# Kernel tuning notes

Hardware: AMD Instinct MI355X
Metric: run time of the kernel (lower is better)

Reference implementation:

```python
import jax, jax.numpy as jnp
import numpy as np

B, CH, N = 131072, 2, 8  # batch, pos/neg channels, coarse graph size
L1, L2 = 64, 32          # latent_gcn, latent2_gcn
NEG_SLOPE = 0.2


def _row_normalize(a):
    # GCN-style row normalization: D^-1 A, zeroing rows with zero sum
    rowsum = a.sum(-1, keepdims=True)
    r_inv = jnp.where(rowsum > 0, 1.0 / rowsum, 0.0)
    return a * r_inv


def _leaky(x):
    return jnp.where(x >= 0, x, NEG_SLOPE * x)


def setup_inputs() -> dict:
    key = jax.random.key(0)
    ks = jax.random.split(key, 16)
    u = lambda k, shape, s: jax.random.uniform(k, shape, jnp.float32, -s, s)
    s1 = 1.0 / np.sqrt(L1)
    s2 = 1.0 / np.sqrt(L2)
    d_in = CH * N * L2            # 512
    d_h1 = N * N                  # 64
    d_h2 = int(N * N * 0.5)       # 32
    return {
        "adj": jax.random.uniform(ks[0], (B, CH, N, N), jnp.float32),
        "Wp1": u(ks[1], (N, L1), s1),  "bp1": u(ks[2], (L1,), s1),
        "Wp2": u(ks[3], (L1, L2), s2), "bp2": u(ks[4], (L2,), s2),
        "Wn1": u(ks[5], (N, L1), s1),  "bn1": u(ks[6], (L1,), s1),
        "Wn2": u(ks[7], (L1, L2), s2), "bn2": u(ks[8], (L2,), s2),
        "Wl1": u(ks[9], (d_in, d_h1), 1.0 / np.sqrt(d_in)),  "bl1": u(ks[10], (d_h1,), 1.0 / np.sqrt(d_in)),
        "Wl2": u(ks[11], (d_h1, d_h2), 1.0 / np.sqrt(d_h1)), "bl2": u(ks[12], (d_h2,), 1.0 / np.sqrt(d_h1)),
        "Wl3": u(ks[13], (d_h2, 1), 1.0 / np.sqrt(d_h2)),    "bl3": u(ks[14], (1,), 1.0 / np.sqrt(d_h2)),
    }


def reference(adj, Wp1, bp1, Wp2, bp2, Wn1, bn1, Wn2, bn2,
              Wl1, bl1, Wl2, bl2, Wl3, bl3):
    # adj: [B, 2, N, N]; channel 0 -> positive GCN, channel 1 -> negative GCN
    Ap = _row_normalize(adj[:, 0])  # [B, N, N]
    An = _row_normalize(adj[:, 1])

    # input features x = eye(N), so eye @ W == W; keep general via broadcast
    def gcn2(A, W1, b1, W2, b2):
        x1 = _leaky(jnp.einsum('bij,jk->bik', A, W1) + b1)        # [B, N, L1]
        x2 = _leaky(jnp.einsum('bij,bjk->bik', A, x1 @ W2) + b2)  # [B, N, L2]
        return x2

    xp = gcn2(Ap, Wp1, bp1, Wp2, bp2)
    xn = gcn2(An, Wn1, bn1, Wn2, bn2)
    x_ = jnp.stack([xp, xn], axis=1)          # [B, 2, N, L2]
    x = x_.reshape(x_.shape[0], -1)           # [B, 2*N*L2]

    h = _leaky(x @ Wl1 + bl1)
    h = _leaky(h @ Wl2 + bl2)
    return h @ Wl3 + bl3                      # [B, 1]
```

## Files before the change

### kernel.cpp

```cpp
#include <hip/hip_runtime.h>

typedef _Float16 f16;
typedef _Float16 f16x2 __attribute__((ext_vector_type(2)));
typedef _Float16 f16x4 __attribute__((ext_vector_type(4)));
typedef _Float16 f16x8 __attribute__((ext_vector_type(8)));
typedef float    f32x4 __attribute__((ext_vector_type(4)));
typedef unsigned int u32;
typedef u32      u32x2 __attribute__((ext_vector_type(2)));
typedef u32      u32x4 __attribute__((ext_vector_type(4)));

#define MFMA32(a, b, c) __builtin_amdgcn_mfma_f32_16x16x32_f16((a), (b), (c), 0, 0, 0)
#define MFMA16(a, b, c) __builtin_amdgcn_mfma_f32_16x16x16f16((a), (b), (c), 0, 0, 0)

__device__ __forceinline__ float leaky(float x) {
    return fmaf(0.4f, __builtin_fabsf(x), 0.6f * x);
}
__device__ __forceinline__ u32 pkrtz(float a, float b) {
    return __builtin_bit_cast(u32, __builtin_amdgcn_cvt_pkrtz(a, b));
}
__device__ __forceinline__ u32 lk_pk2(float a, float b) {
    f16x2 v = __builtin_bit_cast(f16x2, __builtin_amdgcn_cvt_pkrtz(a, b));
    f16x2 z2 = {(f16)0.0f, (f16)0.0f};
    f16x2 mx = __builtin_elementwise_max(v, z2);
    f16x2 mn = __builtin_elementwise_min(v, z2);
    f16x2 r = mn * (f16x2){(f16)0.2f, (f16)0.2f} + mx;
    return __builtin_bit_cast(u32, r);
}
__device__ __forceinline__ f16x4 lk_pk4(const f32x4 z) {
    return __builtin_bit_cast(f16x4, (u32x2){ lk_pk2(z[0], z[1]), lk_pk2(z[2], z[3]) });
}
__device__ __forceinline__ f16x4 pk4(const f32x4 z) {
    return __builtin_bit_cast(f16x4, (u32x2){ pkrtz(z[0], z[1]), pkrtz(z[2], z[3]) });
}
__device__ __forceinline__ void st_lk4(void* p, const f32x4 z) {
    *(u32x2*)p = (u32x2){ lk_pk2(z[0], z[1]), lk_pk2(z[2], z[3]) };
}

__global__ void disc_prepack(const float* __restrict__ Wp1, const float* __restrict__ Wp2,
                             const float* __restrict__ Wn1, const float* __restrict__ Wn2,
                             const float* __restrict__ Wl1, const float* __restrict__ Wl2,
                             f16* __restrict__ ws)
{
    int idx = blockIdx.x * 256 + threadIdx.x;
    if (idx >= 84 * 512 + 24 * 256) return;
    float v = 0.0f;
    if (idx < 84 * 512) {
        int f = idx >> 9, r = idx & 511;
        int lane = r >> 3, e = r & 7;
        int m15 = lane & 15, h = lane >> 4;
        if (f < 64) {
            int mt4 = f >> 4, ks4 = f & 15;
            int k = ks4 * 32 + h * 8 + e;
            v = Wl1[k * 64 + mt4 * 16 + m15];
        } else if (f < 72) {
            int q = f - 64, c = q >> 2, mt = q & 3;
            const float* W1 = c ? Wn1 : Wp1;
            v = (lane < 16) ? W1[e * 64 + mt * 16 + m15] : 0.0f;
        } else if (f < 80) {
            int q = f - 72, c = q >> 2, nt2 = (q >> 1) & 1, ks2 = q & 1;
            const float* W2 = c ? Wn2 : Wp2;
            int k = ks2 * 32 + h * 8 + e;
            v = W2[k * 32 + nt2 * 16 + m15];
        } else {
            int q = f - 80, ms5 = q >> 1, ks5 = q & 1;
            int k = ks5 * 32 + h * 8 + e;
            v = Wl2[k * 32 + ms5 * 16 + m15];
        }
    } else {
        int r2 = idx - 84 * 512;
        int f2 = r2 >> 8, rr = r2 & 255;
        int lane = rr >> 2, e = rr & 3;
        int m15 = lane & 15, h = lane >> 4;
        if (f2 < 16) {
            int c = f2 >> 3, kb = (f2 >> 1) & 3, nt = f2 & 1;
            const float* W2 = c ? Wn2 : Wp2;
            v = W2[(kb * 16 + h * 4 + e) * 32 + nt * 16 + m15];
        } else {
            int q = f2 - 16, kb = q >> 1, nt = q & 1;
            v = Wl2[(kb * 16 + h * 4 + e) * 32 + nt * 16 + m15];
        }
    }
    ws[idx] = (f16)v;
}

__global__ __launch_bounds__(128, 2) void disc_main(
    const float* __restrict__ adj,
    const float* __restrict__ bp1, const float* __restrict__ bp2,
    const float* __restrict__ bn1, const float* __restrict__ bn2,
    const float* __restrict__ bl1, const float* __restrict__ bl2,
    const float* __restrict__ bl3, const float* __restrict__ Wl3,
    const f16* __restrict__ ws, float* __restrict__ out)
{
    extern __shared__ char smem[];
    const int tid  = threadIdx.x;
    const int lane = tid & 63;
    const int wid  = tid >> 6;
    const int h    = lane >> 4;
    const int m15  = lane & 15;
    const int i7   = lane & 7;
    const int r8   = m15 >> 3;

    const f16x8* wsf = (const f16x8*)ws;
    const f16x4* wsq = (const f16x4*)(ws + 84 * 512);
    const int c = wid;

    const f16x8* w1p = wsf + (64 + c * 4) * 64 + lane;
    f16x8 w1t0 = w1p[0], w1t1 = w1p[64], w1t2 = w1p[128], w1t3 = w1p[192];
    const f16x4* w2p = wsq + (c * 8) * 64 + lane;
    f16x4 w2k00 = w2p[0],   w2k01 = w2p[64];
    f16x4 w2k10 = w2p[128], w2k11 = w2p[192];
    f16x4 w2k20 = w2p[256], w2k21 = w2p[320];
    f16x4 w2k30 = w2p[384], w2k31 = w2p[448];
    const f32x4* b1p = (const f32x4*)(c ? bn1 : bp1);
    f32x4 b10 = b1p[h], b11 = b1p[4 + h], b12 = b1p[8 + h], b13 = b1p[12 + h];
    const f32x4* b2p = (const f32x4*)(c ? bn2 : bp2);
    f32x4 b20 = b2p[h], b21 = b2p[4 + h];
    f32x4 bl1v0 = ((const f32x4*)bl1)[h],      bl1v1 = ((const f32x4*)bl1)[4 + h];
    f32x4 bl1v2 = ((const f32x4*)bl1)[8 + h],  bl1v3 = ((const f32x4*)bl1)[12 + h];

    char* wbase = smem + wid * 10240;
    char* Albuf = wbase;
    char* xbuf  = wbase + 2048;
    char* xchg  = smem + 10240;

    const long b0 = (long)blockIdx.x * 16;
    const int rxor = ((m15 >> 1) & 3) << 4;
    const bool bsel = ((h >> 1) == r8);
    const int  hlow = h & 1;
    f32x4 zero4 = {0.0f, 0.0f, 0.0f, 0.0f};
    f16x4 zf4 = {};

    f32x4 a40 = wid ? zero4 : bl1v0;
    f32x4 a41 = wid ? zero4 : bl1v1;
    f32x4 a42 = wid ? zero4 : bl1v2;
    f32x4 a43 = wid ? zero4 : bl1v3;

    #pragma unroll
    for (int q = 0; q < 2; ++q) {
        int rid = q * 64 + lane;
        const f32x4* rp = (const f32x4*)(adj + (b0 + (rid >> 3)) * 128 + c * 64 + (rid & 7) * 8);
        f32x4 a0 = rp[0];
        f32x4 a1 = rp[1];
        float s = ((a0[0] + a0[1]) + (a0[2] + a0[3])) + ((a1[0] + a1[1]) + (a1[2] + a1[3]));
        float rv = (s > 0.0f) ? (1.0f / s) : 0.0f;
        f16x8 row;
        row[0] = (f16)(a0[0] * rv); row[1] = (f16)(a0[1] * rv);
        row[2] = (f16)(a0[2] * rv); row[3] = (f16)(a0[3] * rv);
        row[4] = (f16)(a1[0] * rv); row[5] = (f16)(a1[1] * rv);
        row[6] = (f16)(a1[2] * rv); row[7] = (f16)(a1[3] * rv);
        *(f16x8*)(Albuf + rid * 16) = row;
    }

    #pragma unroll 1
    for (int tp = 0; tp < 4; ++tp) {
        const int ta = tp, tb = tp + 4;
        f16x8 arow_a = *(const f16x8*)(Albuf + (((2 * ta + r8) * 8 + i7) << 4));
        f16x8 arow_b = *(const f16x8*)(Albuf + (((2 * tb + r8) * 8 + i7) << 4));

        f32x4 z0a = MFMA32(w1t0, arow_a, b10);
        f32x4 z1a = MFMA32(w1t1, arow_a, b11);
        f32x4 z2a = MFMA32(w1t2, arow_a, b12);
        f32x4 z3a = MFMA32(w1t3, arow_a, b13);
        f32x4 z0b = MFMA32(w1t0, arow_b, b10);
        f32x4 z1b = MFMA32(w1t1, arow_b, b11);
        f32x4 z2b = MFMA32(w1t2, arow_b, b12);
        f32x4 z3b = MFMA32(w1t3, arow_b, b13);

        f16x4 xa0 = lk_pk4(z0a), xa1 = lk_pk4(z1a), xa2 = lk_pk4(z2a), xa3 = lk_pk4(z3a);
        f16x4 xb0 = lk_pk4(z0b), xb1 = lk_pk4(z1b), xb2 = lk_pk4(z2b), xb3 = lk_pk4(z3b);

        f32x4 y0a = MFMA16(xa0, w2k00, zero4);
        f32x4 y1a = MFMA16(xa0, w2k01, zero4);
        f32x4 y0b = MFMA16(xb0, w2k00, zero4);
        f32x4 y1b = MFMA16(xb0, w2k01, zero4);
        y0a = MFMA16(xa1, w2k10, y0a);
        y1a = MFMA16(xa1, w2k11, y1a);
        y0b = MFMA16(xb1, w2k10, y0b);
        y1b = MFMA16(xb1, w2k11, y1b);
        y0a = MFMA16(xa2, w2k20, y0a);
        y1a = MFMA16(xa2, w2k21, y1a);
        y0b = MFMA16(xb2, w2k20, y0b);
        y1b = MFMA16(xb2, w2k21, y1b);
        y0a = MFMA16(xa3, w2k30, y0a);
        y1a = MFMA16(xa3, w2k31, y1a);
        y0b = MFMA16(xb3, w2k30, y0b);
        y1b = MFMA16(xb3, w2k31, y1b);

        f16x4 pa0 = pk4(y0a), pa1 = pk4(y1a);
        f16x4 pb0 = pk4(y0b), pb1 = pk4(y1b);
        u32x4 ara = __builtin_bit_cast(u32x4, arow_a);
        u32x4 arb = __builtin_bit_cast(u32x4, arow_b);
        f16x4 halfa = __builtin_bit_cast(f16x4,
            hlow ? (u32x2){ara[2], ara[3]} : (u32x2){ara[0], ara[1]});
        f16x4 halfb = __builtin_bit_cast(f16x4,
            hlow ? (u32x2){arb[2], arb[3]} : (u32x2){arb[0], arb[1]});
        f16x4 bfra = bsel ? halfa : zf4;
        f16x4 bfrb = bsel ? halfb : zf4;

        f32x4 x2aa = MFMA16(pa0, bfra, b20);
        f32x4 x2ba = MFMA16(pa1, bfra, b21);
        f32x4 x2ab = MFMA16(pb0, bfrb, b20);
        f32x4 x2bb = MFMA16(pb1, bfrb, b21);

        const int lga = h >> 1;
        const int lgb = (lga + 2) & 3;
        char* fb = xbuf + (i7 << 10);
        {
            int wx = ((ta & 3) ^ i7) << 4;
            int basew = ((2 * ta + r8) << 6) + ((h & 1) << 3);
            st_lk4(fb + ((basew + lga * 16) ^ wx), x2aa);
            st_lk4(fb + ((basew + lgb * 16) ^ wx), x2ba);
        }
        {
            int wx = ((tb & 3) ^ i7) << 4;
            int basew = ((2 * tb + r8) << 6) + ((h & 1) << 3);
            st_lk4(fb + ((basew + lga * 16) ^ wx), x2ab);
            st_lk4(fb + ((basew + lgb * 16) ^ wx), x2bb);
        }
    }

    __builtin_amdgcn_s_setprio(1);
    #pragma unroll 4
    for (int k8 = 0; k8 < 8; ++k8) {
        int xr = rxor ^ (k8 << 4);
        f16x8 xf = *(const f16x8*)(xbuf + (k8 << 10) + ((m15 * 64 + h * 16) ^ xr));
        const f16x8* wl = wsf + (c * 8 + k8) * 64 + lane;
        a40 = MFMA32(wl[0],    xf, a40);
        a41 = MFMA32(wl[1024], xf, a41);
        a42 = MFMA32(wl[2048], xf, a42);
        a43 = MFMA32(wl[3072], xf, a43);
    }
    __builtin_amdgcn_s_setprio(0);

    if (wid == 1) {
        *(f32x4*)(xchg +    0 + lane * 16) = a40;
        *(f32x4*)(xchg + 1024 + lane * 16) = a41;
        *(f32x4*)(xchg + 2048 + lane * 16) = a42;
        *(f32x4*)(xchg + 3072 + lane * 16) = a43;
    }
    __syncthreads();
    if (wid == 0) {
        a40 += *(const f32x4*)(xchg +    0 + lane * 16);
        a41 += *(const f32x4*)(xchg + 1024 + lane * 16);
        a42 += *(const f32x4*)(xchg + 2048 + lane * 16);
        a43 += *(const f32x4*)(xchg + 3072 + lane * 16);

        f16x4 pd0 = lk_pk4(a40), pd1 = lk_pk4(a41);
        f16x4 pd2 = lk_pk4(a42), pd3 = lk_pk4(a43);

        const f16x4* wl2p = wsq + 16 * 64 + lane;
        f16x4 l200 = wl2p[0],   l201 = wl2p[64];
        f16x4 l210 = wl2p[128], l211 = wl2p[192];
        f16x4 l220 = wl2p[256], l221 = wl2p[320];
        f16x4 l230 = wl2p[384], l231 = wl2p[448];
        float c0 = bl2[m15], c1 = bl2[m15 + 16];
        f32x4 a50 = {c0, c0, c0, c0};
        f32x4 a51 = {c1, c1, c1, c1};
        a50 = MFMA16(pd0, l200, a50);
        a51 = MFMA16(pd0, l201, a51);
        a50 = MFMA16(pd1, l210, a50);
        a51 = MFMA16(pd1, l211, a51);
        a50 = MFMA16(pd2, l220, a50);
        a51 = MFMA16(pd2, l221, a51);
        a50 = MFMA16(pd3, l230, a50);
        a51 = MFMA16(pd3, l231, a51);

        float w30 = Wl3[m15], w31 = Wl3[m15 + 16];
        const float bl3s = bl3[0];
        #pragma unroll
        for (int r = 0; r < 4; ++r) {
            float acc = leaky(a50[r]) * w30 + leaky(a51[r]) * w31;
            acc += __shfl_xor(acc, 1);
            acc += __shfl_xor(acc, 2);
            acc += __shfl_xor(acc, 4);
            acc += __shfl_xor(acc, 8);
            if (m15 == 0) out[b0 + h * 4 + r] = acc + bl3s;
        }
    }
}

extern "C" void kernel_launch(void* const* d_in, const int* in_sizes, int n_in,
                              void* d_out, int out_size, void* d_ws, size_t ws_size,
                              hipStream_t stream)
{
    const float* adj  = (const float*)d_in[0];
    const float* Wp1  = (const float*)d_in[1];
    const float* bp1  = (const float*)d_in[2];
    const float* Wp2  = (const float*)d_in[3];
    const float* bp2  = (const float*)d_in[4];
    const float* Wn1  = (const float*)d_in[5];
    const float* bn1  = (const float*)d_in[6];
    const float* Wn2  = (const float*)d_in[7];
    const float* bn2  = (const float*)d_in[8];
    const float* Wl1  = (const float*)d_in[9];
    const float* bl1  = (const float*)d_in[10];
    const float* Wl2  = (const float*)d_in[11];
    const float* bl2  = (const float*)d_in[12];
    const float* Wl3  = (const float*)d_in[13];
    const float* bl3  = (const float*)d_in[14];
    f16* ws = (f16*)d_ws;
    float* out = (float*)d_out;

    hipLaunchKernelGGL(disc_prepack, dim3(192), dim3(256), 0, stream,
                       Wp1, Wp2, Wn1, Wn2, Wl1, Wl2, ws);

    const int ldsBytes = 20480;
    hipFuncSetAttribute(reinterpret_cast<const void*>(disc_main),
                        hipFuncAttributeMaxDynamicSharedMemorySize, ldsBytes);
    hipLaunchKernelGGL(disc_main, dim3(8192), dim3(128), ldsBytes, stream,
                       adj, bp1, bp2, bn1, bn2, bl1, bl2, bl3, Wl3, ws, out);
}
```

Before: 54.74 us.

## Split each channel's work across two waves with four-way cross-wave reduction

Doubles the block to 256 threads so each adjacency channel is handled by two waves. Each wave normalizes half the rows, runs half the GCN tiles and does half of the K-loop of the first dense layer. Partial accumulators from three waves are then reduced through LDS by wave 0. This adds two extra barriers and more LDS reduction traffic in exchange for more waves in flight and shorter per-wave serial chains. The reciprocal is also switched to the hardware rcp approximation.

```diff
diff --git a/kernel.cpp b/kernel.cpp
--- a/kernel.cpp
+++ b/kernel.cpp
@@ -83,7 +83,7 @@
     ws[idx] = (f16)v;
 }
 
-__global__ __launch_bounds__(128, 2) void disc_main(
+__global__ __launch_bounds__(256, 8) void disc_main(
     const float* __restrict__ adj,
     const float* __restrict__ bp1, const float* __restrict__ bp2,
     const float* __restrict__ bn1, const float* __restrict__ bn2,
@@ -95,6 +95,8 @@
     const int tid  = threadIdx.x;
     const int lane = tid & 63;
     const int wid  = tid >> 6;
+    const int c    = wid >> 1;
+    const int half = wid & 1;
     const int h    = lane >> 4;
     const int m15  = lane & 15;
     const int i7   = lane & 7;
@@ -102,7 +104,6 @@
 
     const f16x8* wsf = (const f16x8*)ws;
     const f16x4* wsq = (const f16x4*)(ws + 84 * 512);
-    const int c = wid;
 
     const f16x8* w1p = wsf + (64 + c * 4) * 64 + lane;
     f16x8 w1t0 = w1p[0], w1t1 = w1p[64], w1t2 = w1p[128], w1t3 = w1p[192];
@@ -115,13 +116,10 @@
     f32x4 b10 = b1p[h], b11 = b1p[4 + h], b12 = b1p[8 + h], b13 = b1p[12 + h];
     const f32x4* b2p = (const f32x4*)(c ? bn2 : bp2);
     f32x4 b20 = b2p[h], b21 = b2p[4 + h];
-    f32x4 bl1v0 = ((const f32x4*)bl1)[h],      bl1v1 = ((const f32x4*)bl1)[4 + h];
-    f32x4 bl1v2 = ((const f32x4*)bl1)[8 + h],  bl1v3 = ((const f32x4*)bl1)[12 + h];
-
-    char* wbase = smem + wid * 10240;
-    char* Albuf = wbase;
-    char* xbuf  = wbase + 2048;
-    char* xchg  = smem + 10240;
+
+    char* Albuf = smem + wid * 1024;
+    char* xbuf  = smem + 4096 + c * 8192;
+    char* xchg  = smem;
 
     const long b0 = (long)blockIdx.x * 16;
     const int rxor = ((m15 >> 1) & 3) << 4;
@@ -130,32 +128,28 @@
     f32x4 zero4 = {0.0f, 0.0f, 0.0f, 0.0f};
     f16x4 zf4 = {};
 
-    f32x4 a40 = wid ? zero4 : bl1v0;
-    f32x4 a41 = wid ? zero4 : bl1v1;
-    f32x4 a42 = wid ? zero4 : bl1v2;
-    f32x4 a43 = wid ? zero4 : bl1v3;
-
-    #pragma unroll
-    for (int q = 0; q < 2; ++q) {
-        int rid = q * 64 + lane;
+    {
+        const int rid = half * 64 + lane;
         const f32x4* rp = (const f32x4*)(adj + (b0 + (rid >> 3)) * 128 + c * 64 + (rid & 7) * 8);
         f32x4 a0 = rp[0];
         f32x4 a1 = rp[1];
         float s = ((a0[0] + a0[1]) + (a0[2] + a0[3])) + ((a1[0] + a1[1]) + (a1[2] + a1[3]));
-        float rv = (s > 0.0f) ? (1.0f / s) : 0.0f;
+        float rv = (s > 0.0f) ? __builtin_amdgcn_rcpf(s) : 0.0f;
         f16x8 row;
         row[0] = (f16)(a0[0] * rv); row[1] = (f16)(a0[1] * rv);
         row[2] = (f16)(a0[2] * rv); row[3] = (f16)(a0[3] * rv);
         row[4] = (f16)(a1[0] * rv); row[5] = (f16)(a1[1] * rv);
         row[6] = (f16)(a1[2] * rv); row[7] = (f16)(a1[3] * rv);
-        *(f16x8*)(Albuf + rid * 16) = row;
+        *(f16x8*)(Albuf + lane * 16) = row;
     }
 
     #pragma unroll 1
-    for (int tp = 0; tp < 4; ++tp) {
-        const int ta = tp, tb = tp + 4;
-        f16x8 arow_a = *(const f16x8*)(Albuf + (((2 * ta + r8) * 8 + i7) << 4));
-        f16x8 arow_b = *(const f16x8*)(Albuf + (((2 * tb + r8) * 8 + i7) << 4));
+    for (int tp = 0; tp < 2; ++tp) {
+        const int tla = tp, tlb = tp + 2;
+        const int ta = half * 4 + tla;
+        const int tb = half * 4 + tlb;
+        f16x8 arow_a = *(const f16x8*)(Albuf + (((2 * tla + r8) * 8 + i7) << 4));
+        f16x8 arow_b = *(const f16x8*)(Albuf + (((2 * tlb + r8) * 8 + i7) << 4));
 
         f32x4 z0a = MFMA32(w1t0, arow_a, b10);
         f32x4 z1a = MFMA32(w1t1, arow_a, b11);
@@ -219,9 +213,20 @@
         }
     }
 
+    __syncthreads();
+
+    f32x4 a40 = zero4, a41 = zero4, a42 = zero4, a43 = zero4;
+    if (wid == 0) {
+        a40 = ((const f32x4*)bl1)[h];
+        a41 = ((const f32x4*)bl1)[4 + h];
+        a42 = ((const f32x4*)bl1)[8 + h];
+        a43 = ((const f32x4*)bl1)[12 + h];
+    }
     __builtin_amdgcn_s_setprio(1);
-    #pragma unroll 4
-    for (int k8 = 0; k8 < 8; ++k8) {
+    const int kbase = half * 4;
+    #pragma unroll
+    for (int kq = 0; kq < 4; ++kq) {
+        const int k8 = kbase + kq;
         int xr = rxor ^ (k8 << 4);
         f16x8 xf = *(const f16x8*)(xbuf + (k8 << 10) + ((m15 * 64 + h * 16) ^ xr));
         const f16x8* wl = wsf + (c * 8 + k8) * 64 + lane;
@@ -232,18 +237,24 @@
     }
     __builtin_amdgcn_s_setprio(0);
 
-    if (wid == 1) {
-        *(f32x4*)(xchg +    0 + lane * 16) = a40;
-        *(f32x4*)(xchg + 1024 + lane * 16) = a41;
-        *(f32x4*)(xchg + 2048 + lane * 16) = a42;
-        *(f32x4*)(xchg + 3072 + lane * 16) = a43;
+    __syncthreads();
+    if (wid) {
+        char* dst = xchg + (wid - 1) * 4096 + lane * 16;
+        *(f32x4*)(dst +    0) = a40;
+        *(f32x4*)(dst + 1024) = a41;
+        *(f32x4*)(dst + 2048) = a42;
+        *(f32x4*)(dst + 3072) = a43;
     }
     __syncthreads();
     if (wid == 0) {
-        a40 += *(const f32x4*)(xchg +    0 + lane * 16);
-        a41 += *(const f32x4*)(xchg + 1024 + lane * 16);
-        a42 += *(const f32x4*)(xchg + 2048 + lane * 16);
-        a43 += *(const f32x4*)(xchg + 3072 + lane * 16);
+        #pragma unroll
+        for (int p = 0; p < 3; ++p) {
+            const f32x4* xp = (const f32x4*)(xchg + p * 4096 + lane * 16);
+            a40 += xp[0];
+            a41 += xp[64];
+            a42 += xp[128];
+            a43 += xp[192];
+        }
 
         f16x4 pd0 = lk_pk4(a40), pd1 = lk_pk4(a41);
         f16x4 pd2 = lk_pk4(a42), pd3 = lk_pk4(a43);
@@ -307,6 +318,6 @@
     const int ldsBytes = 20480;
     hipFuncSetAttribute(reinterpret_cast<const void*>(disc_main),
                         hipFuncAttributeMaxDynamicSharedMemorySize, ldsBytes);
-    hipLaunchKernelGGL(disc_main, dim3(8192), dim3(128), ldsBytes, stream,
+    hipLaunchKernelGGL(disc_main, dim3(8192), dim3(256), ldsBytes, stream,
                        adj, bp1, bp2, bn1, bn2, bl1, bl2, bl3, Wl3, ws, out);
 }
```

Result: slower. 175.6 us (+220.9%).

## Make blocks persistent over 8 tiles with register prefetch of next adjacency tile

Applied to the files above, without the earlier changes.

Each block now processes 8 batch tiles of 16 in a loop instead of one, loading the next tile's adjacency rows into registers while the current tile's GCN and MLP compute runs. Per-block weight and bias loads, including the final-layer weights now hoisted out of the loop, are amortised over more work. The exchange buffer moves to its own LDS region and a second barrier is added to protect it between tiles. The grid shrinks to 1024 blocks, so fewer waves are available to hide latency. Reciprocal uses the fast rcp intrinsic.

```diff
diff --git a/kernel.cpp b/kernel.cpp
--- a/kernel.cpp
+++ b/kernel.cpp
@@ -11,6 +11,8 @@
 
 #define MFMA32(a, b, c) __builtin_amdgcn_mfma_f32_16x16x32_f16((a), (b), (c), 0, 0, 0)
 #define MFMA16(a, b, c) __builtin_amdgcn_mfma_f32_16x16x16f16((a), (b), (c), 0, 0, 0)
+
+#define TILES 8
 
 __device__ __forceinline__ float leaky(float x) {
     return fmaf(0.4f, __builtin_fabsf(x), 0.6f * x);
@@ -118,164 +120,204 @@
     f32x4 bl1v0 = ((const f32x4*)bl1)[h],      bl1v1 = ((const f32x4*)bl1)[4 + h];
     f32x4 bl1v2 = ((const f32x4*)bl1)[8 + h],  bl1v3 = ((const f32x4*)bl1)[12 + h];
 
+    f16x4 l200, l201, l210, l211, l220, l221, l230, l231;
+    float c0 = 0.0f, c1 = 0.0f, w30 = 0.0f, w31 = 0.0f, bl3s = 0.0f;
+    if (wid == 0) {
+        const f16x4* wl2p = wsq + 16 * 64 + lane;
+        l200 = wl2p[0];   l201 = wl2p[64];
+        l210 = wl2p[128]; l211 = wl2p[192];
+        l220 = wl2p[256]; l221 = wl2p[320];
+        l230 = wl2p[384]; l231 = wl2p[448];
+        c0 = bl2[m15]; c1 = bl2[m15 + 16];
+        w30 = Wl3[m15]; w31 = Wl3[m15 + 16];
+        bl3s = bl3[0];
+    }
+
     char* wbase = smem + wid * 10240;
     char* Albuf = wbase;
     char* xbuf  = wbase + 2048;
-    char* xchg  = smem + 10240;
-
-    const long b0 = (long)blockIdx.x * 16;
+    char* xchg  = smem + 20480;
+
     const int rxor = ((m15 >> 1) & 3) << 4;
     const bool bsel = ((h >> 1) == r8);
     const int  hlow = h & 1;
     f32x4 zero4 = {0.0f, 0.0f, 0.0f, 0.0f};
     f16x4 zf4 = {};
 
-    f32x4 a40 = wid ? zero4 : bl1v0;
-    f32x4 a41 = wid ? zero4 : bl1v1;
-    f32x4 a42 = wid ? zero4 : bl1v2;
-    f32x4 a43 = wid ? zero4 : bl1v3;
-
-    #pragma unroll
-    for (int q = 0; q < 2; ++q) {
-        int rid = q * 64 + lane;
-        const f32x4* rp = (const f32x4*)(adj + (b0 + (rid >> 3)) * 128 + c * 64 + (rid & 7) * 8);
-        f32x4 a0 = rp[0];
-        f32x4 a1 = rp[1];
-        float s = ((a0[0] + a0[1]) + (a0[2] + a0[3])) + ((a1[0] + a1[1]) + (a1[2] + a1[3]));
-        float rv = (s > 0.0f) ? (1.0f / s) : 0.0f;
-        f16x8 row;
-        row[0] = (f16)(a0[0] * rv); row[1] = (f16)(a0[1] * rv);
-        row[2] = (f16)(a0[2] * rv); row[3] = (f16)(a0[3] * rv);
-        row[4] = (f16)(a1[0] * rv); row[5] = (f16)(a1[1] * rv);
-        row[6] = (f16)(a1[2] * rv); row[7] = (f16)(a1[3] * rv);
-        *(f16x8*)(Albuf + rid * 16) = row;
+    long b0 = (long)blockIdx.x * (16 * TILES);
+
+    f32x4 c00, c01, c10, c11;
+    {
+        const f32x4* rp0 = (const f32x4*)(adj + (b0 + (lane >> 3)) * 128 + c * 64 + (lane & 7) * 8);
+        c00 = rp0[0]; c01 = rp0[1];
+        const int rid1 = 64 + lane;
+        const f32x4* rp1 = (const f32x4*)(adj + (b0 + (rid1 >> 3)) * 128 + c * 64 + (rid1 & 7) * 8);
+        c10 = rp1[0]; c11 = rp1[1];
     }
 
     #pragma unroll 1
-    for (int tp = 0; tp < 4; ++tp) {
-        const int ta = tp, tb = tp + 4;
-        f16x8 arow_a = *(const f16x8*)(Albuf + (((2 * ta + r8) * 8 + i7) << 4));
-        f16x8 arow_b = *(const f16x8*)(Albuf + (((2 * tb + r8) * 8 + i7) << 4));
-
-        f32x4 z0a = MFMA32(w1t0, arow_a, b10);
-        f32x4 z1a = MFMA32(w1t1, arow_a, b11);
-        f32x4 z2a = MFMA32(w1t2, arow_a, b12);
-        f32x4 z3a = MFMA32(w1t3, arow_a, b13);
-        f32x4 z0b = MFMA32(w1t0, arow_b, b10);
-        f32x4 z1b = MFMA32(w1t1, arow_b, b11);
-        f32x4 z2b = MFMA32(w1t2, arow_b, b12);
-        f32x4 z3b = MFMA32(w1t3, arow_b, b13);
-
-        f16x4 xa0 = lk_pk4(z0a), xa1 = lk_pk4(z1a), xa2 = lk_pk4(z2a), xa3 = lk_pk4(z3a);
-        f16x4 xb0 = lk_pk4(z0b), xb1 = lk_pk4(z1b), xb2 = lk_pk4(z2b), xb3 = lk_pk4(z3b);
-
-        f32x4 y0a = MFMA16(xa0, w2k00, zero4);
-        f32x4 y1a = MFMA16(xa0, w2k01, zero4);
-        f32x4 y0b = MFMA16(xb0, w2k00, zero4);
-        f32x4 y1b = MFMA16(xb0, w2k01, zero4);
-        y0a = MFMA16(xa1, w2k10, y0a);
-        y1a = MFMA16(xa1, w2k11, y1a);
-        y0b = MFMA16(xb1, w2k10, y0b);
-        y1b = MFMA16(xb1, w2k11, y1b);
-        y0a = MFMA16(xa2, w2k20, y0a);
-        y1a = MFMA16(xa2, w2k21, y1a);
-        y0b = MFMA16(xb2, w2k20, y0b);
-        y1b = MFMA16(xb2, w2k21, y1b);
-        y0a = MFMA16(xa3, w2k30, y0a);
-        y1a = MFMA16(xa3, w2k31, y1a);
-        y0b = MFMA16(xb3, w2k30, y0b);
-        y1b = MFMA16(xb3, w2k31, y1b);
-
-        f16x4 pa0 = pk4(y0a), pa1 = pk4(y1a);
-        f16x4 pb0 = pk4(y0b), pb1 = pk4(y1b);
-        u32x4 ara = __builtin_bit_cast(u32x4, arow_a);
-        u32x4 arb = __builtin_bit_cast(u32x4, arow_b);
-        f16x4 halfa = __builtin_bit_cast(f16x4,
-            hlow ? (u32x2){ara[2], ara[3]} : (u32x2){ara[0], ara[1]});
-        f16x4 halfb = __builtin_bit_cast(f16x4,
-            hlow ? (u32x2){arb[2], arb[3]} : (u32x2){arb[0], arb[1]});
-        f16x4 bfra = bsel ? halfa : zf4;
-        f16x4 bfrb = bsel ? halfb : zf4;
-
-        f32x4 x2aa = MFMA16(pa0, bfra, b20);
-        f32x4 x2ba = MFMA16(pa1, bfra, b21);
-        f32x4 x2ab = MFMA16(pb0, bfrb, b20);
-        f32x4 x2bb = MFMA16(pb1, bfrb, b21);
-
-        const int lga = h >> 1;
-        const int lgb = (lga + 2) & 3;
-        char* fb = xbuf + (i7 << 10);
+    for (int it = 0; it < TILES; ++it, b0 += 16) {
         {
-            int wx = ((ta & 3) ^ i7) << 4;
-            int basew = ((2 * ta + r8) << 6) + ((h & 1) << 3);
-            st_lk4(fb + ((basew + lga * 16) ^ wx), x2aa);
-            st_lk4(fb + ((basew + lgb * 16) ^ wx), x2ba);
+            float s = ((c00[0] + c00[1]) + (c00[2] + c00[3])) + ((c01[0] + c01[1]) + (c01[2] + c01[3]));
+            float rv = (s > 0.0f) ? __builtin_amdgcn_rcpf(s) : 0.0f;
+            f16x8 row;
+            row[0] = (f16)(c00[0] * rv); row[1] = (f16)(c00[1] * rv);
+            row[2] = (f16)(c00[2] * rv); row[3] = (f16)(c00[3] * rv);
+            row[4] = (f16)(c01[0] * rv); row[5] = (f16)(c01[1] * rv);
+            row[6] = (f16)(c01[2] * rv); row[7] = (f16)(c01[3] * rv);
+            *(f16x8*)(Albuf + lane * 16) = row;
         }
         {
-            int wx = ((tb & 3) ^ i7) << 4;
-            int basew = ((2 * tb + r8) << 6) + ((h & 1) << 3);
-            st_lk4(fb + ((basew + lga * 16) ^ wx), x2ab);
-            st_lk4(fb + ((basew + lgb * 16) ^ wx), x2bb);
-        }
-    }
-
-    __builtin_amdgcn_s_setprio(1);
-    #pragma unroll 4
-    for (int k8 = 0; k8 < 8; ++k8) {
-        int xr = rxor ^ (k8 << 4);
-        f16x8 xf = *(const f16x8*)(xbuf + (k8 << 10) + ((m15 * 64 + h * 16) ^ xr));
-        const f16x8* wl = wsf + (c * 8 + k8) * 64 + lane;
-        a40 = MFMA32(wl[0],    xf, a40);
-        a41 = MFMA32(wl[1024], xf, a41);
-        a42 = MFMA32(wl[2048], xf, a42);
-        a43 = MFMA32(wl[3072], xf, a43);
-    }
-    __builtin_amdgcn_s_setprio(0);
-
-    if (wid == 1) {
-        *(f32x4*)(xchg +    0 + lane * 16) = a40;
-        *(f32x4*)(xchg + 1024 + lane * 16) = a41;
-        *(f32x4*)(xchg + 2048 + lane * 16) = a42;
-        *(f32x4*)(xchg + 3072 + lane * 16) = a43;
-    }
-    __syncthreads();
-    if (wid == 0) {
-        a40 += *(const f32x4*)(xchg +    0 + lane * 16);
-        a41 += *(const f32x4*)(xchg + 1024 + lane * 16);
-        a42 += *(const f32x4*)(xchg + 2048 + lane * 16);
-        a43 += *(const f32x4*)(xchg + 3072 + lane * 16);
-
-        f16x4 pd0 = lk_pk4(a40), pd1 = lk_pk4(a41);
-        f16x4 pd2 = lk_pk4(a42), pd3 = lk_pk4(a43);
-
-        const f16x4* wl2p = wsq + 16 * 64 + lane;
-        f16x4 l200 = wl2p[0],   l201 = wl2p[64];
-        f16x4 l210 = wl2p[128], l211 = wl2p[192];
-        f16x4 l220 = wl2p[256], l221 = wl2p[320];
-        f16x4 l230 = wl2p[384], l231 = wl2p[448];
-        float c0 = bl2[m15], c1 = bl2[m15 + 16];
-        f32x4 a50 = {c0, c0, c0, c0};
-        f32x4 a51 = {c1, c1, c1, c1};
-        a50 = MFMA16(pd0, l200, a50);
-        a51 = MFMA16(pd0, l201, a51);
-        a50 = MFMA16(pd1, l210, a50);
-        a51 = MFMA16(pd1, l211, a51);
-        a50 = MFMA16(pd2, l220, a50);
-        a51 = MFMA16(pd2, l221, a51);
-        a50 = MFMA16(pd3, l230, a50);
-        a51 = MFMA16(pd3, l231, a51);
-
-        float w30 = Wl3[m15], w31 = Wl3[m15 + 16];
-        const float bl3s = bl3[0];
-        #pragma unroll
-        for (int r = 0; r < 4; ++r) {
-            float acc = leaky(a50[r]) * w30 + leaky(a51[r]) * w31;
-            acc += __shfl_xor(acc, 1);
-            acc += __shfl_xor(acc, 2);
-            acc += __shfl_xor(acc, 4);
-            acc += __shfl_xor(acc, 8);
-            if (m15 == 0) out[b0 + h * 4 + r] = acc + bl3s;
-        }
+            float s = ((c10[0] + c10[1]) + (c10[2] + c10[3])) + ((c11[0] + c11[1]) + (c11[2] + c11[3]));
+            float rv = (s > 0.0f) ? __builtin_amdgcn_rcpf(s) : 0.0f;
+            f16x8 row;
+            row[0] = (f16)(c10[0] * rv); row[1] = (f16)(c10[1] * rv);
+            row[2] = (f16)(c10[2] * rv); row[3] = (f16)(c10[3] * rv);
+            row[4] = (f16)(c11[0] * rv); row[5] = (f16)(c11[1] * rv);
+            row[6] = (f16)(c11[2] * rv); row[7] = (f16)(c11[3] * rv);
+            *(f16x8*)(Albuf + (64 + lane) * 16) = row;
+        }
+
+        f32x4 n00, n01, n10, n11;
+        const bool more = (it + 1 < TILES);
+        if (more) {
+            const f32x4* rp0 = (const f32x4*)(adj + (b0 + 16 + (lane >> 3)) * 128 + c * 64 + (lane & 7) * 8);
+            n00 = rp0[0]; n01 = rp0[1];
+            const int rid1 = 64 + lane;
+            const f32x4* rp1 = (const f32x4*)(adj + (b0 + 16 + (rid1 >> 3)) * 128 + c * 64 + (rid1 & 7) * 8);
+            n10 = rp1[0]; n11 = rp1[1];
+        }
+
+        #pragma unroll 1
+        for (int tp = 0; tp < 4; ++tp) {
+            const int ta = tp, tb = tp + 4;
+            f16x8 arow_a = *(const f16x8*)(Albuf + (((2 * ta + r8) * 8 + i7) << 4));
+            f16x8 arow_b = *(const f16x8*)(Albuf + (((2 * tb + r8) * 8 + i7) << 4));
+
+            f32x4 z0a = MFMA32(w1t0, arow_a, b10);
+            f32x4 z1a = MFMA32(w1t1, arow_a, b11);
+            f32x4 z2a = MFMA32(w1t2, arow_a, b12);
+            f32x4 z3a = MFMA32(w1t3, arow_a, b13);
+            f32x4 z0b = MFMA32(w1t0, arow_b, b10);
+            f32x4 z1b = MFMA32(w1t1, arow_b, b11);
+            f32x4 z2b = MFMA32(w1t2, arow_b, b12);
+            f32x4 z3b = MFMA32(w1t3, arow_b, b13);
+
+            f16x4 xa0 = lk_pk4(z0a), xa1 = lk_pk4(z1a), xa2 = lk_pk4(z2a), xa3 = lk_pk4(z3a);
+            f16x4 xb0 = lk_pk4(z0b), xb1 = lk_pk4(z1b), xb2 = lk_pk4(z2b), xb3 = lk_pk4(z3b);
+
+            f32x4 y0a = MFMA16(xa0, w2k00, zero4);
+            f32x4 y1a = MFMA16(xa0, w2k01, zero4);
+            f32x4 y0b = MFMA16(xb0, w2k00, zero4);
+            f32x4 y1b = MFMA16(xb0, w2k01, zero4);
+            y0a = MFMA16(xa1, w2k10, y0a);
+            y1a = MFMA16(xa1, w2k11, y1a);
+            y0b = MFMA16(xb1, w2k10, y0b);
+            y1b = MFMA16(xb1, w2k11, y1b);
+            y0a = MFMA16(xa2, w2k20, y0a);
+            y1a = MFMA16(xa2, w2k21, y1a);
+            y0b = MFMA16(xb2, w2k20, y0b);
+            y1b = MFMA16(xb2, w2k21, y1b);
+            y0a = MFMA16(xa3, w2k30, y0a);
+            y1a = MFMA16(xa3, w2k31, y1a);
+            y0b = MFMA16(xb3, w2k30, y0b);
+            y1b = MFMA16(xb3, w2k31, y1b);
+
+            f16x4 pa0 = pk4(y0a), pa1 = pk4(y1a);
+            f16x4 pb0 = pk4(y0b), pb1 = pk4(y1b);
+            u32x4 ara = __builtin_bit_cast(u32x4, arow_a);
+            u32x4 arb = __builtin_bit_cast(u32x4, arow_b);
+            f16x4 halfa = __builtin_bit_cast(f16x4,
+                hlow ? (u32x2){ara[2], ara[3]} : (u32x2){ara[0], ara[1]});
+            f16x4 halfb = __builtin_bit_cast(f16x4,
+                hlow ? (u32x2){arb[2], arb[3]} : (u32x2){arb[0], arb[1]});
+            f16x4 bfra = bsel ? halfa : zf4;
+            f16x4 bfrb = bsel ? halfb : zf4;
+
+            f32x4 x2aa = MFMA16(pa0, bfra, b20);
+            f32x4 x2ba = MFMA16(pa1, bfra, b21);
+            f32x4 x2ab = MFMA16(pb0, bfrb, b20);
+            f32x4 x2bb = MFMA16(pb1, bfrb, b21);
+
+            const int lga = h >> 1;
+            const int lgb = (lga + 2) & 3;
+            char* fb = xbuf + (i7 << 10);
+            {
+                int wx = ((ta & 3) ^ i7) << 4;
+                int basew = ((2 * ta + r8) << 6) + ((h & 1) << 3);
+                st_lk4(fb + ((basew + lga * 16) ^ wx), x2aa);
+                st_lk4(fb + ((basew + lgb * 16) ^ wx), x2ba);
+            }
+            {
+                int wx = ((tb & 3) ^ i7) << 4;
+                int basew = ((2 * tb + r8) << 6) + ((h & 1) << 3);
+                st_lk4(fb + ((basew + lga * 16) ^ wx), x2ab);
+                st_lk4(fb + ((basew + lgb * 16) ^ wx), x2bb);
+            }
+        }
+
+        f32x4 a40 = wid ? zero4 : bl1v0;
+        f32x4 a41 = wid ? zero4 : bl1v1;
+        f32x4 a42 = wid ? zero4 : bl1v2;
+        f32x4 a43 = wid ? zero4 : bl1v3;
+        __builtin_amdgcn_s_setprio(1);
+        #pragma unroll 4
+        for (int k8 = 0; k8 < 8; ++k8) {
+            int xr = rxor ^ (k8 << 4);
+            f16x8 xf = *(const f16x8*)(xbuf + (k8 << 10) + ((m15 * 64 + h * 16) ^ xr));
+            const f16x8* wl = wsf + (c * 8 + k8) * 64 + lane;
+            a40 = MFMA32(wl[0],    xf, a40);
+            a41 = MFMA32(wl[1024], xf, a41);
+            a42 = MFMA32(wl[2048], xf, a42);
+            a43 = MFMA32(wl[3072], xf, a43);
+        }
+        __builtin_amdgcn_s_setprio(0);
+
+        if (wid == 1) {
+            *(f32x4*)(xchg +    0 + lane * 16) = a40;
+            *(f32x4*)(xchg + 1024 + lane * 16) = a41;
+            *(f32x4*)(xchg + 2048 + lane * 16) = a42;
+            *(f32x4*)(xchg + 3072 + lane * 16) = a43;
+        }
+        __syncthreads();
+        f32x4 p0, p1, p2, p3;
+        if (wid == 0) {
+            p0 = *(const f32x4*)(xchg +    0 + lane * 16);
+            p1 = *(const f32x4*)(xchg + 1024 + lane * 16);
+            p2 = *(const f32x4*)(xchg + 2048 + lane * 16);
+            p3 = *(const f32x4*)(xchg + 3072 + lane * 16);
+        }
+        __syncthreads();
+
+        if (wid == 0) {
+            a40 += p0; a41 += p1; a42 += p2; a43 += p3;
+
+            f16x4 pd0 = lk_pk4(a40), pd1 = lk_pk4(a41);
+            f16x4 pd2 = lk_pk4(a42), pd3 = lk_pk4(a43);
+
+            f32x4 a50 = {c0, c0, c0, c0};
+            f32x4 a51 = {c1, c1, c1, c1};
+            a50 = MFMA16(pd0, l200, a50);
+            a51 = MFMA16(pd0, l201, a51);
+            a50 = MFMA16(pd1, l210, a50);
+            a51 = MFMA16(pd1, l211, a51);
+            a50 = MFMA16(pd2, l220, a50);
+            a51 = MFMA16(pd2, l221, a51);
+            a50 = MFMA16(pd3, l230, a50);
+            a51 = MFMA16(pd3, l231, a51);
+
+            #pragma unroll
+            for (int r = 0; r < 4; ++r) {
+                float acc = leaky(a50[r]) * w30 + leaky(a51[r]) * w31;
+                acc += __shfl_xor(acc, 1);
+                acc += __shfl_xor(acc, 2);
+                acc += __shfl_xor(acc, 4);
+                acc += __shfl_xor(acc, 8);
+                if (m15 == 0) out[b0 + h * 4 + r] = acc + bl3s;
+            }
+        }
+
+        if (more) { c00 = n00; c01 = n01; c10 = n10; c11 = n11; }
     }
 }
 
@@ -304,9 +346,9 @@
     hipLaunchKernelGGL(disc_prepack, dim3(192), dim3(256), 0, stream,
                        Wp1, Wp2, Wn1, Wn2, Wl1, Wl2, ws);
 
-    const int ldsBytes = 20480;
+    const int ldsBytes = 24576;
     hipFuncSetAttribute(reinterpret_cast<const void*>(disc_main),
                         hipFuncAttributeMaxDynamicSharedMemorySize, ldsBytes);
-    hipLaunchKernelGGL(disc_main, dim3(8192), dim3(128), ldsBytes, stream,
+    hipLaunchKernelGGL(disc_main, dim3(8192 / TILES), dim3(128), ldsBytes, stream,
                        adj, bp1, bp2, bn1, bn2, bl1, bl2, bl3, Wl3, ws, out);
 }
```

Result: no change. 54.37 us (-0.7%).

## Use single-wave blocks processing both channels over four batch tiles

Applied to the files above, without the earlier changes.

Restructures the main kernel from two-wave blocks (one wave per channel, combined through LDS and a barrier) to one wave that processes both channels sequentially and loops over four 16-sample tiles. All weights and biases, including the second dense layer, are loaded into registers once per block. This removes the cross-wave exchange and the __syncthreads, and also switches to rcp and a cheaper max-based leaky relu. The catch is much higher register pressure from holding both channels' weights, serial channel processing within a wave, and a grid of only 2048 single-wave blocks, which may reduce latency hiding.

```diff
diff --git a/kernel.cpp b/kernel.cpp
--- a/kernel.cpp
+++ b/kernel.cpp
@@ -12,6 +12,8 @@
 #define MFMA32(a, b, c) __builtin_amdgcn_mfma_f32_16x16x32_f16((a), (b), (c), 0, 0, 0)
 #define MFMA16(a, b, c) __builtin_amdgcn_mfma_f32_16x16x16f16((a), (b), (c), 0, 0, 0)
 
+#define TILES 4
+
 __device__ __forceinline__ float leaky(float x) {
     return fmaf(0.4f, __builtin_fabsf(x), 0.6f * x);
 }
@@ -20,10 +22,8 @@
 }
 __device__ __forceinline__ u32 lk_pk2(float a, float b) {
     f16x2 v = __builtin_bit_cast(f16x2, __builtin_amdgcn_cvt_pkrtz(a, b));
-    f16x2 z2 = {(f16)0.0f, (f16)0.0f};
-    f16x2 mx = __builtin_elementwise_max(v, z2);
-    f16x2 mn = __builtin_elementwise_min(v, z2);
-    f16x2 r = mn * (f16x2){(f16)0.2f, (f16)0.2f} + mx;
+    f16x2 s = v * (f16x2){(f16)0.2f, (f16)0.2f};
+    f16x2 r = __builtin_elementwise_max(v, s);
     return __builtin_bit_cast(u32, r);
 }
 __device__ __forceinline__ f16x4 lk_pk4(const f32x4 z) {
@@ -83,7 +83,7 @@
     ws[idx] = (f16)v;
 }
 
-__global__ __launch_bounds__(128, 2) void disc_main(
+__global__ __launch_bounds__(64, 2) void disc_main(
     const float* __restrict__ adj,
     const float* __restrict__ bp1, const float* __restrict__ bp2,
     const float* __restrict__ bn1, const float* __restrict__ bn2,
@@ -92,9 +92,7 @@
     const f16* __restrict__ ws, float* __restrict__ out)
 {
     extern __shared__ char smem[];
-    const int tid  = threadIdx.x;
-    const int lane = tid & 63;
-    const int wid  = tid >> 6;
+    const int lane = threadIdx.x;
     const int h    = lane >> 4;
     const int m15  = lane & 15;
     const int i7   = lane & 7;
@@ -102,158 +100,152 @@
 
     const f16x8* wsf = (const f16x8*)ws;
     const f16x4* wsq = (const f16x4*)(ws + 84 * 512);
-    const int c = wid;
-
-    const f16x8* w1p = wsf + (64 + c * 4) * 64 + lane;
-    f16x8 w1t0 = w1p[0], w1t1 = w1p[64], w1t2 = w1p[128], w1t3 = w1p[192];
-    const f16x4* w2p = wsq + (c * 8) * 64 + lane;
-    f16x4 w2k00 = w2p[0],   w2k01 = w2p[64];
-    f16x4 w2k10 = w2p[128], w2k11 = w2p[192];
-    f16x4 w2k20 = w2p[256], w2k21 = w2p[320];
-    f16x4 w2k30 = w2p[384], w2k31 = w2p[448];
-    const f32x4* b1p = (const f32x4*)(c ? bn1 : bp1);
-    f32x4 b10 = b1p[h], b11 = b1p[4 + h], b12 = b1p[8 + h], b13 = b1p[12 + h];
-    const f32x4* b2p = (const f32x4*)(c ? bn2 : bp2);
-    f32x4 b20 = b2p[h], b21 = b2p[4 + h];
+
+    const f16x8* w1pp = wsf + 64 * 64 + lane;
+    f16x8 Wp10 = w1pp[0], Wp11 = w1pp[64], Wp12 = w1pp[128], Wp13 = w1pp[192];
+    const f16x4* w2pp = wsq + lane;
+    f16x4 Kp00 = w2pp[0],   Kp01 = w2pp[64];
+    f16x4 Kp10 = w2pp[128], Kp11 = w2pp[192];
+    f16x4 Kp20 = w2pp[256], Kp21 = w2pp[320];
+    f16x4 Kp30 = w2pp[384], Kp31 = w2pp[448];
+    const f32x4* b1pp = (const f32x4*)bp1;
+    f32x4 Bp10 = b1pp[h], Bp11 = b1pp[4 + h], Bp12 = b1pp[8 + h], Bp13 = b1pp[12 + h];
+    const f32x4* b2pp = (const f32x4*)bp2;
+    f32x4 Bp20 = b2pp[h], Bp21 = b2pp[4 + h];
+
+    const f16x8* w1pn = wsf + (64 + 4) * 64 + lane;
+    f16x8 Wn10 = w1pn[0], Wn11 = w1pn[64], Wn12 = w1pn[128], Wn13 = w1pn[192];
+    const f16x4* w2pn = wsq + 8 * 64 + lane;
+    f16x4 Kn00 = w2pn[0],   Kn01 = w2pn[64];
+    f16x4 Kn10 = w2pn[128], Kn11 = w2pn[192];
+    f16x4 Kn20 = w2pn[256], Kn21 = w2pn[320];
+    f16x4 Kn30 = w2pn[384], Kn31 = w2pn[448];
+    const f32x4* b1pn = (const f32x4*)bn1;
+    f32x4 Bn10 = b1pn[h], Bn11 = b1pn[4 + h], Bn12 = b1pn[8 + h], Bn13 = b1pn[12 + h];
+    const f32x4* b2pn = (const f32x4*)bn2;
+    f32x4 Bn20 = b2pn[h], Bn21 = b2pn[4 + h];
+
     f32x4 bl1v0 = ((const f32x4*)bl1)[h],      bl1v1 = ((const f32x4*)bl1)[4 + h];
     f32x4 bl1v2 = ((const f32x4*)bl1)[8 + h],  bl1v3 = ((const f32x4*)bl1)[12 + h];
-
-    char* wbase = smem + wid * 10240;
-    char* Albuf = wbase;
-    char* xbuf  = wbase + 2048;
-    char* xchg  = smem + 10240;
-
-    const long b0 = (long)blockIdx.x * 16;
+    const f16x4* wl2p = wsq + 16 * 64 + lane;
+    f16x4 l200 = wl2p[0],   l201 = wl2p[64];
+    f16x4 l210 = wl2p[128], l211 = wl2p[192];
+    f16x4 l220 = wl2p[256], l221 = wl2p[320];
+    f16x4 l230 = wl2p[384], l231 = wl2p[448];
+    float c0 = bl2[m15], c1 = bl2[m15 + 16];
+    float w30 = Wl3[m15], w31 = Wl3[m15 + 16];
+    const float bl3s = bl3[0];
+
+    char* Albuf = smem;
+    char* xbuf  = smem + 2048;
+
     const int rxor = ((m15 >> 1) & 3) << 4;
     const bool bsel = ((h >> 1) == r8);
     const int  hlow = h & 1;
     f32x4 zero4 = {0.0f, 0.0f, 0.0f, 0.0f};
     f16x4 zf4 = {};
 
-    f32x4 a40 = wid ? zero4 : bl1v0;
-    f32x4 a41 = wid ? zero4 : bl1v1;
-    f32x4 a42 = wid ? zero4 : bl1v2;
-    f32x4 a43 = wid ? zero4 : bl1v3;
-
-    #pragma unroll
-    for (int q = 0; q < 2; ++q) {
-        int rid = q * 64 + lane;
-        const f32x4* rp = (const f32x4*)(adj + (b0 + (rid >> 3)) * 128 + c * 64 + (rid & 7) * 8);
-        f32x4 a0 = rp[0];
-        f32x4 a1 = rp[1];
-        float s = ((a0[0] + a0[1]) + (a0[2] + a0[3])) + ((a1[0] + a1[1]) + (a1[2] + a1[3]));
-        float rv = (s > 0.0f) ? (1.0f / s) : 0.0f;
-        f16x8 row;
-        row[0] = (f16)(a0[0] * rv); row[1] = (f16)(a0[1] * rv);
-        row[2] = (f16)(a0[2] * rv); row[3] = (f16)(a0[3] * rv);
-        row[4] = (f16)(a1[0] * rv); row[5] = (f16)(a1[1] * rv);
-        row[6] = (f16)(a1[2] * rv); row[7] = (f16)(a1[3] * rv);
-        *(f16x8*)(Albuf + rid * 16) = row;
-    }
+    auto run_channel = [&](long b0, int c,
+        f16x8 W10, f16x8 W11, f16x8 W12, f16x8 W13,
+        f16x4 K00, f16x4 K01, f16x4 K10, f16x4 K11,
+        f16x4 K20, f16x4 K21, f16x4 K30, f16x4 K31,
+        f32x4 B10, f32x4 B11, f32x4 B12, f32x4 B13,
+        f32x4 B20, f32x4 B21,
+        f32x4& a40, f32x4& a41, f32x4& a42, f32x4& a43)
+    {
+        {
+            const f32x4* rp0 = (const f32x4*)(adj + (b0 + (lane >> 3)) * 128 + c * 64 + (lane & 7) * 8);
+            const f32x4* rp1 = (const f32x4*)(adj + (b0 + 8 + (lane >> 3)) * 128 + c * 64 + (lane & 7) * 8);
+            f32x4 a0 = rp0[0], a1 = rp0[1];
+            f32x4 b0v = rp1[0], b1v = rp1[1];
+            {
+                float s = ((a0[0] + a0[1]) + (a0[2] + a0[3])) + ((a1[0] + a1[1]) + (a1[2] + a1[3]));
+                float rv = (s > 0.0f) ? __builtin_amdgcn_rcpf(s) : 0.0f;
+                u32x4 row = { pkrtz(a0[0] * rv, a0[1] * rv), pkrtz(a0[2] * rv, a0[3] * rv),
+                              pkrtz(a1[0] * rv, a1[1] * rv), pkrtz(a1[2] * rv, a1[3] * rv) };
+                *(u32x4*)(Albuf + lane * 16) = row;
+            }
+            {
+                float s = ((b0v[0] + b0v[1]) + (b0v[2] + b0v[3])) + ((b1v[0] + b1v[1]) + (b1v[2] + b1v[3]));
+                float rv = (s > 0.0f) ? __builtin_amdgcn_rcpf(s) : 0.0f;
+                u32x4 row = { pkrtz(b0v[0] * rv, b0v[1] * rv), pkrtz(b0v[2] * rv, b0v[3] * rv),
+                              pkrtz(b1v[0] * rv, b1v[1] * rv), pkrtz(b1v[2] * rv, b1v[3] * rv) };
+                *(u32x4*)(Albuf + (64 + lane) * 16) = row;
+            }
+        }
+
+        #pragma unroll
+        for (int t = 0; t < 8; ++t) {
+            f16x8 arow = *(const f16x8*)(Albuf + (((2 * t + r8) * 8 + i7) << 4));
+
+            f32x4 z0 = MFMA32(W10, arow, B10);
+            f32x4 z1 = MFMA32(W11, arow, B11);
+            f32x4 z2 = MFMA32(W12, arow, B12);
+            f32x4 z3 = MFMA32(W13, arow, B13);
+
+            f16x4 x0 = lk_pk4(z0), x1 = lk_pk4(z1), x2 = lk_pk4(z2), x3 = lk_pk4(z3);
+
+            f32x4 y0 = MFMA16(x0, K00, zero4);
+            f32x4 y1 = MFMA16(x0, K01, zero4);
+            y0 = MFMA16(x1, K10, y0);
+            y1 = MFMA16(x1, K11, y1);
+            y0 = MFMA16(x2, K20, y0);
+            y1 = MFMA16(x2, K21, y1);
+            y0 = MFMA16(x3, K30, y0);
+            y1 = MFMA16(x3, K31, y1);
+
+            f16x4 pa0 = pk4(y0), pa1 = pk4(y1);
+            u32x4 ar = __builtin_bit_cast(u32x4, arow);
+            f16x4 halfa = __builtin_bit_cast(f16x4,
+                hlow ? (u32x2){ar[2], ar[3]} : (u32x2){ar[0], ar[1]});
+            f16x4 bfra = bsel ? halfa : zf4;
+
+            f32x4 x2a = MFMA16(pa0, bfra, B20);
+            f32x4 x2b = MFMA16(pa1, bfra, B21);
+
+            const int lga = h >> 1;
+            const int lgb = lga ^ 2;
+            char* fb = xbuf + (i7 << 10);
+            int wx = ((t & 3) ^ i7) << 4;
+            int basew = ((2 * t + r8) << 6) + ((h & 1) << 3);
+            st_lk4(fb + ((basew + lga * 16) ^ wx), x2a);
+            st_lk4(fb + ((basew + lgb * 16) ^ wx), x2b);
+        }
+
+        __builtin_amdgcn_s_setprio(1);
+        #pragma unroll
+        for (int k8 = 0; k8 < 8; ++k8) {
+            int xr = rxor ^ (k8 << 4);
+            f16x8 xf = *(const f16x8*)(xbuf + (k8 << 10) + ((m15 * 64 + h * 16) ^ xr));
+            const f16x8* wl = wsf + (c * 8 + k8) * 64 + lane;
+            a40 = MFMA32(wl[0],    xf, a40);
+            a41 = MFMA32(wl[1024], xf, a41);
+            a42 = MFMA32(wl[2048], xf, a42);
+            a43 = MFMA32(wl[3072], xf, a43);
+        }
+        __builtin_amdgcn_s_setprio(0);
+    };
+
+    long b0 = (long)blockIdx.x * (16 * TILES);
 
     #pragma unroll 1
-    for (int tp = 0; tp < 4; ++tp) {
-        const int ta = tp, tb = tp + 4;
-        f16x8 arow_a = *(const f16x8*)(Albuf + (((2 * ta + r8) * 8 + i7) << 4));
-        f16x8 arow_b = *(const f16x8*)(Albuf + (((2 * tb + r8) * 8 + i7) << 4));
-
-        f32x4 z0a = MFMA32(w1t0, arow_a, b10);
-        f32x4 z1a = MFMA32(w1t1, arow_a, b11);
-        f32x4 z2a = MFMA32(w1t2, arow_a, b12);
-        f32x4 z3a = MFMA32(w1t3, arow_a, b13);
-        f32x4 z0b = MFMA32(w1t0, arow_b, b10);
-        f32x4 z1b = MFMA32(w1t1, arow_b, b11);
-        f32x4 z2b = MFMA32(w1t2, arow_b, b12);
-        f32x4 z3b = MFMA32(w1t3, arow_b, b13);
-
-        f16x4 xa0 = lk_pk4(z0a), xa1 = lk_pk4(z1a), xa2 = lk_pk4(z2a), xa3 = lk_pk4(z3a);
-        f16x4 xb0 = lk_pk4(z0b), xb1 = lk_pk4(z1b), xb2 = lk_pk4(z2b), xb3 = lk_pk4(z3b);
-
-        f32x4 y0a = MFMA16(xa0, w2k00, zero4);
-        f32x4 y1a = MFMA16(xa0, w2k01, zero4);
-        f32x4 y0b = MFMA16(xb0, w2k00, zero4);
-        f32x4 y1b = MFMA16(xb0, w2k01, zero4);
-        y0a = MFMA16(xa1, w2k10, y0a);
-        y1a = MFMA16(xa1, w2k11, y1a);
-        y0b = MFMA16(xb1, w2k10, y0b);
-        y1b = MFMA16(xb1, w2k11, y1b);
-        y0a = MFMA16(xa2, w2k20, y0a);
-        y1a = MFMA16(xa2, w2k21, y1a);
-        y0b = MFMA16(xb2, w2k20, y0b);
-        y1b = MFMA16(xb2, w2k21, y1b);
-        y0a = MFMA16(xa3, w2k30, y0a);
-        y1a = MFMA16(xa3, w2k31, y1a);
-        y0b = MFMA16(xb3, w2k30, y0b);
-        y1b = MFMA16(xb3, w2k31, y1b);
-
-        f16x4 pa0 = pk4(y0a), pa1 = pk4(y1a);
-        f16x4 pb0 = pk4(y0b), pb1 = pk4(y1b);
-        u32x4 ara = __builtin_bit_cast(u32x4, arow_a);
-        u32x4 arb = __builtin_bit_cast(u32x4, arow_b);
-        f16x4 halfa = __builtin_bit_cast(f16x4,
-            hlow ? (u32x2){ara[2], ara[3]} : (u32x2){ara[0], ara[1]});
-        f16x4 halfb = __builtin_bit_cast(f16x4,
-            hlow ? (u32x2){arb[2], arb[3]} : (u32x2){arb[0], arb[1]});
-        f16x4 bfra = bsel ? halfa : zf4;
-        f16x4 bfrb = bsel ? halfb : zf4;
-
-        f32x4 x2aa = MFMA16(pa0, bfra, b20);
-        f32x4 x2ba = MFMA16(pa1, bfra, b21);
-        f32x4 x2ab = MFMA16(pb0, bfrb, b20);
-        f32x4 x2bb = MFMA16(pb1, bfrb, b21);
-
-        const int lga = h >> 1;
-        const int lgb = (lga + 2) & 3;
-        char* fb = xbuf + (i7 << 10);
-        {
-            int wx = ((ta & 3) ^ i7) << 4;
-            int basew = ((2 * ta + r8) << 6) + ((h & 1) << 3);
-            st_lk4(fb + ((basew + lga * 16) ^ wx), x2aa);
-            st_lk4(fb + ((basew + lgb * 16) ^ wx), x2ba);
-        }
-        {
-            int wx = ((tb & 3) ^ i7) << 4;
-            int basew = ((2 * tb + r8) << 6) + ((h & 1) << 3);
-            st_lk4(fb + ((basew + lga * 16) ^ wx), x2ab);
-            st_lk4(fb + ((basew + lgb * 16) ^ wx), x2bb);
-        }
-    }
-
-    __builtin_amdgcn_s_setprio(1);
-    #pragma unroll 4
-    for (int k8 = 0; k8 < 8; ++k8) {
-        int xr = rxor ^ (k8 << 4);
-        f16x8 xf = *(const f16x8*)(xbuf + (k8 << 10) + ((m15 * 64 + h * 16) ^ xr));
-        const f16x8* wl = wsf + (c * 8 + k8) * 64 + lane;
-        a40 = MFMA32(wl[0],    xf, a40);
-        a41 = MFMA32(wl[1024], xf, a41);
-        a42 = MFMA32(wl[2048], xf, a42);
-        a43 = MFMA32(wl[3072], xf, a43);
-    }
-    __builtin_amdgcn_s_setprio(0);
-
-    if (wid == 1) {
-        *(f32x4*)(xchg +    0 + lane * 16) = a40;
-        *(f32x4*)(xchg + 1024 + lane * 16) = a41;
-        *(f32x4*)(xchg + 2048 + lane * 16) = a42;
-        *(f32x4*)(xchg + 3072 + lane * 16) = a43;
-    }
-    __syncthreads();
-    if (wid == 0) {
-        a40 += *(const f32x4*)(xchg +    0 + lane * 16);
-        a41 += *(const f32x4*)(xchg + 1024 + lane * 16);
-        a42 += *(const f32x4*)(xchg + 2048 + lane * 16);
-        a43 += *(const f32x4*)(xchg + 3072 + lane * 16);
+    for (int it = 0; it < TILES; ++it, b0 += 16) {
+        f32x4 a40 = bl1v0, a41 = bl1v1, a42 = bl1v2, a43 = bl1v3;
+
+        run_channel(b0, 0,
+                    Wp10, Wp11, Wp12, Wp13,
+                    Kp00, Kp01, Kp10, Kp11, Kp20, Kp21, Kp30, Kp31,
+                    Bp10, Bp11, Bp12, Bp13, Bp20, Bp21,
+                    a40, a41, a42, a43);
+        run_channel(b0, 1,
+                    Wn10, Wn11, Wn12, Wn13,
+                    Kn00, Kn01, Kn10, Kn11, Kn20, Kn21, Kn30, Kn31,
+                    Bn10, Bn11, Bn12, Bn13, Bn20, Bn21,
+                    a40, a41, a42, a43);
 
         f16x4 pd0 = lk_pk4(a40), pd1 = lk_pk4(a41);
         f16x4 pd2 = lk_pk4(a42), pd3 = lk_pk4(a43);
 
-        const f16x4* wl2p = wsq + 16 * 64 + lane;
-        f16x4 l200 = wl2p[0],   l201 = wl2p[64];
-        f16x4 l210 = wl2p[128], l211 = wl2p[192];
-        f16x4 l220 = wl2p[256], l221 = wl2p[320];
-        f16x4 l230 = wl2p[384], l231 = wl2p[448];
-        float c0 = bl2[m15], c1 = bl2[m15 + 16];
         f32x4 a50 = {c0, c0, c0, c0};
         f32x4 a51 = {c1, c1, c1, c1};
         a50 = MFMA16(pd0, l200, a50);
@@ -265,8 +257,6 @@
         a50 = MFMA16(pd3, l230, a50);
         a51 = MFMA16(pd3, l231, a51);
 
-        float w30 = Wl3[m15], w31 = Wl3[m15 + 16];
-        const float bl3s = bl3[0];
         #pragma unroll
         for (int r = 0; r < 4; ++r) {
             float acc = leaky(a50[r]) * w30 + leaky(a51[r]) * w31;
@@ -304,9 +294,9 @@
     hipLaunchKernelGGL(disc_prepack, dim3(192), dim3(256), 0, stream,
                        Wp1, Wp2, Wn1, Wn2, Wl1, Wl2, ws);
 
-    const int ldsBytes = 20480;
+    const int ldsBytes = 10240;
     hipFuncSetAttribute(reinterpret_cast<const void*>(disc_main),
                         hipFuncAttributeMaxDynamicSharedMemorySize, ldsBytes);
-    hipLaunchKernelGGL(disc_main, dim3(8192), dim3(128), ldsBytes, stream,
+    hipLaunchKernelGGL(disc_main, dim3(8192 / TILES), dim3(64), ldsBytes, stream,
                        adj, bp1, bp2, bn1, bn2, bl1, bl2, bl3, Wl3, ws, out);
 }
```

New measurement: 155.5 us. +184.1%, slower.
